# Performance work log

Hardware: AMD Instinct MI355X
Metric: run time of the kernel (lower is better)

## Reference

```python
import jax, jax.numpy as jnp
import numpy as np

B, T, C, H = 4, 4096, 2048, 128


def setup_inputs() -> dict:
    key = jax.random.key(0)
    ks = jax.random.split(key, 7)
    s = 0.02
    return {
        "x": jax.random.normal(ks[0], (B, T, C), dtype=jnp.float32),
        "Wk": jax.random.normal(ks[1], (C, H), dtype=jnp.float32) * s,
        "bk": jax.random.normal(ks[2], (H,), dtype=jnp.float32) * s,
        "Wq": jax.random.normal(ks[3], (C, H), dtype=jnp.float32) * s,
        "bq": jax.random.normal(ks[4], (H,), dtype=jnp.float32) * s,
        "Wv": jax.random.normal(ks[5], (C, H), dtype=jnp.float32) * s,
        "bv": jax.random.normal(ks[6], (H,), dtype=jnp.float32) * s,
    }


def reference(x, Wk, bk, Wq, bq, Wv, bv):
    # x: [B, T, C]
    Bq, Tq, Cq = x.shape
    k = x @ Wk + bk  # [B, T, H]
    q = x @ Wq + bq
    v = x @ Wv + bv
    # NOTE: original scales by C**-0.5 (input emb dim), faithfully reproduced.
    scale = jnp.asarray(Cq, x.dtype) ** -0.5
    wei = jnp.einsum("bth,bsh->bts", q, k) * scale  # [B, T, T]
    causal = jnp.tril(jnp.ones((Tq, Tq), dtype=bool))
    wei = jnp.where(causal, wei, -jnp.inf)
    wei = jax.nn.softmax(wei, axis=-1)
    # dropout omitted (inference/eval mode)
    return jnp.einsum("bts,bsh->bth", wei, v)  # [B, T, H]
```

## Files before the change

kernel.cpp:

```cpp
#include <hip/hip_runtime.h>
#include <hip/hip_bf16.h>
#include <stdint.h>

#define T_SEQ 4096
#define C_DIM 2048
#define H_DIM 128
#define NBATCH 4

typedef unsigned short u16;
typedef __attribute__((ext_vector_type(8))) __bf16 bf16x8;
typedef __attribute__((ext_vector_type(4))) float f32x4;
typedef __attribute__((ext_vector_type(8))) unsigned short u16x8;

__device__ __forceinline__ u16 f2bf(float f) {
  union { float f; uint32_t i; } v; v.f = f;
  uint32_t r = v.i + 0x7FFFu + ((v.i >> 16) & 1u);
  return (u16)(r >> 16);
}

__device__ __forceinline__ void gload16(const void* g, void* l) {
  __builtin_amdgcn_global_load_lds(
      (__attribute__((address_space(1))) void*)(g),
      (__attribute__((address_space(3))) void*)(l), 16, 0, 0);
}

__device__ __forceinline__ f32x4 mfma_bf16(bf16x8 a, bf16x8 b, f32x4 c) {
  return __builtin_amdgcn_mfma_f32_16x16x32_bf16(a, b, c, 0, 0, 0);
}

template<int CTRL>
__device__ __forceinline__ float dpp_mov(float x) {
  return __int_as_float(__builtin_amdgcn_mov_dpp(__float_as_int(x), CTRL, 0xF, 0xF, true));
}
__device__ __forceinline__ float red16_max(float v) {
  v = fmaxf(v, dpp_mov<0x121>(v));
  v = fmaxf(v, dpp_mov<0x122>(v));
  v = fmaxf(v, dpp_mov<0x124>(v));
  v = fmaxf(v, dpp_mov<0x128>(v));
  return v;
}
__device__ __forceinline__ float red16_sum(float v) {
  v += dpp_mov<0x121>(v);
  v += dpp_mov<0x122>(v);
  v += dpp_mov<0x124>(v);
  v += dpp_mov<0x128>(v);
  return v;
}

__global__ __launch_bounds__(256) void transpose_w(
    const float* __restrict__ Wq, const float* __restrict__ Wk,
    const float* __restrict__ Wv, u16* __restrict__ Wt)
{
  __shared__ u16 Wl[64 * 72];
  const int bk = blockIdx.x;
  const int bn = blockIdx.y;
  const int p  = blockIdx.z;
  const float* W = (p == 0) ? Wq : (p == 1) ? Wk : Wv;
  const int t = threadIdx.x;

  for (int ps = 0; ps < 16; ++ps) {
    int e  = ps * 256 + t;
    int kk = e >> 6, nn = e & 63;
    Wl[kk * 72 + nn] = f2bf(W[(size_t)(bk * 64 + kk) * H_DIM + bn * 64 + nn]);
  }
  __syncthreads();
  for (int ps = 0; ps < 16; ++ps) {
    int o  = ps * 256 + t;
    int nl = o >> 6, kl = o & 63;
    int n  = bn * 64 + nl;
    int g  = kl >> 3, j = kl & 7;
    int ks = ((g ^ (n & 7)) << 3) | j;
    Wt[(size_t)p * (H_DIM * C_DIM) + (size_t)n * C_DIM + bk * 64 + kl] = Wl[ks * 72 + nl];
  }
}

__global__ __launch_bounds__(256, 2) void qkv_gemm(
    const float* __restrict__ x, const u16* __restrict__ Wt,
    const float* __restrict__ bq, const float* __restrict__ bk, const float* __restrict__ bv,
    u16* __restrict__ qo, u16* __restrict__ ko, u16* __restrict__ vTo)
{
  __shared__ alignas(16) u16 SMEM[128 * 128];
  u16* As = SMEM;
  u16* Bs = SMEM + 128 * 64;

  const int tid  = threadIdx.x;
  const int w    = tid >> 6, lane = tid & 63;
  const int t16  = lane & 15, quad = lane >> 4;
  const int wr   = w >> 1, wc = w & 1;
  const int rt   = blockIdx.x;
  const int p    = blockIdx.y;

  const u16*   Wp = Wt + (size_t)p * (H_DIM * C_DIM);
  const float* bp = (p == 0) ? bq : (p == 1) ? bk : bv;

  f32x4 acc[4][4];
  for (int i = 0; i < 4; ++i)
    for (int j = 0; j < 4; ++j) acc[i][j] = f32x4{0.f, 0.f, 0.f, 0.f};

  const size_t rowBase = (size_t)rt * 128;

  for (int k0 = 0; k0 < C_DIM; k0 += 64) {
    __syncthreads();
    for (int j = 0; j < 4; ++j) {
      int e8 = (((j << 2) + w) * 64 + lane) * 8;
      int rr = e8 >> 6, kk = e8 & 63;
      gload16(Wp + (size_t)rr * C_DIM + k0 + kk, &Bs[e8]);
    }
    for (int ps = 0; ps < 4; ++ps) {
      int gidx = ps * 256 + tid;
      int row = gidx >> 3, g = gidx & 7;
      const float4* xp = (const float4*)&x[(rowBase + row) * C_DIM + k0 + g * 8];
      float4 a0 = xp[0], a1 = xp[1];
      u16x8 pk;
      pk[0] = f2bf(a0.x); pk[1] = f2bf(a0.y); pk[2] = f2bf(a0.z); pk[3] = f2bf(a0.w);
      pk[4] = f2bf(a1.x); pk[5] = f2bf(a1.y); pk[6] = f2bf(a1.z); pk[7] = f2bf(a1.w);
      *(u16x8*)&As[row * 64 + ((g ^ (row & 7)) << 3)] = pk;
    }
    __syncthreads();
    for (int ks = 0; ks < 2; ++ks) {
      bf16x8 af[4], bfr[4];
      for (int ra = 0; ra < 4; ++ra)
        af[ra] = *(const bf16x8*)&As[(wr * 64 + ra * 16 + t16) * 64 +
                                     (((ks * 4 + quad) ^ (t16 & 7)) << 3)];
      for (int cb = 0; cb < 4; ++cb)
        bfr[cb] = *(const bf16x8*)&Bs[(wc * 64 + cb * 16 + t16) * 64 +
                                      (((ks * 4 + quad) ^ (t16 & 7)) << 3)];
      for (int ra = 0; ra < 4; ++ra)
        for (int cb = 0; cb < 4; ++cb)
          acc[ra][cb] = mfma_bf16(af[ra], bfr[cb], acc[ra][cb]);
    }
  }

  __syncthreads();
  for (int cb = 0; cb < 4; ++cb) {
    int col = wc * 64 + cb * 16 + t16;
    float bias = bp[col];
    for (int ra = 0; ra < 4; ++ra) {
      for (int r = 0; r < 4; ++r) {
        int row16 = wr * 64 + ra * 16 + quad * 4 + r;
        float v = acc[ra][cb][r] + bias;
        if (p == 2) {
          int swz = (row16 >> 3) ^ (col & 15);
          SMEM[col * 128 + (swz << 3) + (row16 & 7)] = f2bf(v);
        } else {
          int g = col >> 3;
          SMEM[row16 * 128 + (((g ^ (row16 & 15)) << 3) | (col & 7))] = f2bf(v);
        }
      }
    }
  }
  __syncthreads();

  if (p == 1) {
    u16* kдst = ko + rowBase * H_DIM;
    for (int ps = 0; ps < 8; ++ps) {
      int c = ps * 256 + tid;
      *(u16x8*)&kдst[c * 8] = *(const u16x8*)&SMEM[c * 8];
    }
  } else if (p == 0) {
    for (int ps = 0; ps < 8; ++ps) {
      int c = ps * 256 + tid;
      int row16 = c >> 4, g = c & 15;
      u16x8 v = *(const u16x8*)&SMEM[row16 * 128 + ((g ^ (row16 & 15)) << 3)];
      *(u16x8*)&qo[(rowBase + row16) * H_DIM + g * 8] = v;
    }
  } else {
    const int bb = rt >> 5;
    const int tb = (rt & 31) * 128;
    for (int ps = 0; ps < 8; ++ps) {
      int c = ps * 256 + tid;
      int d = c >> 4, gt = c & 15;
      u16x8 v = *(const u16x8*)&SMEM[d * 128 + ((gt ^ (d & 15)) << 3)];
      int toff = tb + ((gt >> 3) << 6) + (((gt & 7) ^ (d & 7)) << 3);
      *(u16x8*)&vTo[((size_t)bb * H_DIM + d) * T_SEQ + toff] = v;
    }
  }
}

__global__ __launch_bounds__(256, 2) void flash_attn(
    const u16* __restrict__ q, const u16* __restrict__ k,
    const u16* __restrict__ vT, float* __restrict__ out,
    float* __restrict__ Opart, float* __restrict__ MLpart, int split)
{
  __shared__ alignas(16) u16 Kt[2][64 * 128];
  __shared__ alignas(16) u16 Vt[2][128 * 64];
  __shared__ alignas(16) u16 Ps[4 * 16 * 72];

  const int tid  = threadIdx.x;
  const int w    = tid >> 6, lane = tid & 63;
  const int t16  = lane & 15, quad = lane >> 4;
  const int b    = blockIdx.x;

  int qt, kt0, ktn, slot;
  if (split) {
    int bid = blockIdx.y;
    if (bid < 32)      { qt = 32 + bid; kt0 = 0;  ktn = 32;      slot = (b * 32 + bid) * 2; }
    else if (bid < 64) { qt = 95 - bid; kt0 = 32; ktn = qt - 31; slot = (b * 32 + (qt - 32)) * 2 + 1; }
    else               { qt = 95 - bid; kt0 = 0;  ktn = qt + 1;  slot = -1; }
  } else {
    qt = 63 - blockIdx.y; kt0 = 0; ktn = qt + 1; slot = -1;
  }

  const float SCALE = 0.022097086912079612f;
  const float L2E   = 1.4426950408889634f;

  bf16x8 qf[4];
  {
    const u16* qrow = q + ((size_t)(b * T_SEQ + qt * 64 + w * 16 + t16)) * H_DIM;
    for (int c = 0; c < 4; ++c)
      qf[c] = *(const bf16x8*)(qrow + c * 32 + quad * 8);
  }

  f32x4 Oc[8];
  for (int i = 0; i < 8; ++i) Oc[i] = f32x4{0.f, 0.f, 0.f, 0.f};
  float mrow[4] = {-1e30f, -1e30f, -1e30f, -1e30f};
  float lrow[4] = {0.f, 0.f, 0.f, 0.f};

  const u16* kbase = k  + ((size_t)b * T_SEQ) * H_DIM;
  const u16* vbase = vT + ((size_t)b * H_DIM) * T_SEQ;

  {
    const u16* kg = kbase + (size_t)(kt0 * 64) * H_DIM;
    for (int j = 0; j < 4; ++j) {
      int e8 = (((j << 2) + w) * 64 + lane) * 8;
      gload16(kg + e8, &Kt[0][e8]);
      int d = e8 >> 6, kk = e8 & 63;
      gload16(vbase + (size_t)d * T_SEQ + kt0 * 64 + kk, &Vt[0][e8]);
    }
  }

  int cur = 0;
  for (int it = 0; it < ktn; ++it) {
    const int kt = kt0 + it;
    __syncthreads();
    if (it + 1 < ktn) {
      const int nb = cur ^ 1, ktn1 = kt + 1;
      const u16* kg = kbase + (size_t)(ktn1 * 64) * H_DIM;
      for (int j = 0; j < 4; ++j) {
        int e8 = (((j << 2) + w) * 64 + lane) * 8;
        gload16(kg + e8, &Kt[nb][e8]);
        int d = e8 >> 6, kk = e8 & 63;
        gload16(vbase + (size_t)d * T_SEQ + ktn1 * 64 + kk, &Vt[nb][e8]);
      }
    }

    f32x4 S[4];
    for (int ct = 0; ct < 4; ++ct) S[ct] = f32x4{0.f, 0.f, 0.f, 0.f};
    for (int c = 0; c < 4; ++c) {
      for (int ct = 0; ct < 4; ++ct) {
        bf16x8 kf = *(const bf16x8*)&Kt[cur][(ct * 16 + t16) * H_DIM +
                                            (((c * 4 + quad) ^ t16) << 3)];
        S[ct] = mfma_bf16(qf[c], kf, S[ct]);
      }
    }

    const bool diag = (kt == qt);
    for (int ct = 0; ct < 4; ++ct)
      for (int r = 0; r < 4; ++r) {
        float s = S[ct][r] * SCALE;
        if (diag && (ct * 16 + t16 > w * 16 + quad * 4 + r)) s = -1e30f;
        S[ct][r] = s;
      }

    float alpha[4], mnew[4];
    for (int r = 0; r < 4; ++r) {
      float mx = red16_max(fmaxf(fmaxf(S[0][r], S[1][r]), fmaxf(S[2][r], S[3][r])));
      mnew[r]  = fmaxf(mrow[r], mx);
      alpha[r] = exp2f((mrow[r] - mnew[r]) * L2E);
      mrow[r]  = mnew[r];
    }
    for (int r = 0; r < 4; ++r) {
      float s = 0.f;
      for (int ct = 0; ct < 4; ++ct) {
        float pv = exp2f((S[ct][r] - mnew[r]) * L2E);
        S[ct][r] = pv;
        s += pv;
      }
      lrow[r] = lrow[r] * alpha[r] + red16_sum(s);
    }
    for (int dt = 0; dt < 8; ++dt)
      for (int r = 0; r < 4; ++r)
        Oc[dt][r] *= alpha[r];

    u16* pw = &Ps[w * 1152];
    for (int ct = 0; ct < 4; ++ct)
      for (int r = 0; r < 4; ++r)
        pw[(quad * 4 + r) * 72 + ct * 16 + t16] = f2bf(S[ct][r]);
    __asm__ volatile("s_waitcnt lgkmcnt(0)" ::: "memory");

    for (int ks = 0; ks < 2; ++ks) {
      bf16x8 pf = *(const bf16x8*)&pw[t16 * 72 + ks * 32 + quad * 8];
      for (int dt = 0; dt < 8; ++dt) {
        bf16x8 vf = *(const bf16x8*)&Vt[cur][(dt * 16 + t16) * 64 +
                                            (((ks * 4 + quad) ^ (t16 & 7)) << 3)];
        Oc[dt] = mfma_bf16(pf, vf, Oc[dt]);
      }
    }
    cur ^= 1;
  }

  if (slot < 0) {
    for (int r = 0; r < 4; ++r) {
      float inv = 1.0f / lrow[r];
      size_t row = (size_t)b * T_SEQ + qt * 64 + w * 16 + quad * 4 + r;
      for (int dt = 0; dt < 8; ++dt)
        out[row * H_DIM + dt * 16 + t16] = Oc[dt][r] * inv;
    }
  } else {
    if (t16 == 0) {
      for (int r = 0; r < 4; ++r) {
        int row = w * 16 + quad * 4 + r;
        MLpart[(size_t)slot * 128 + row * 2 + 0] = mrow[r];
        MLpart[(size_t)slot * 128 + row * 2 + 1] = lrow[r];
      }
    }
    float* op = Opart + (size_t)slot * 8192;
    for (int r = 0; r < 4; ++r) {
      int row = w * 16 + quad * 4 + r;
      for (int dt = 0; dt < 8; ++dt)
        op[row * 128 + dt * 16 + t16] = Oc[dt][r];
    }
  }
}

__global__ __launch_bounds__(256) void combine(
    const float* __restrict__ Opart, const float* __restrict__ MLpart,
    float* __restrict__ out)
{
  __shared__ float c1s[64], c2s[64];
  const float L2E = 1.4426950408889634f;
  const int s = blockIdx.x;
  const int b = s >> 5, qt = 32 + (s & 31);
  const int t = threadIdx.x;

  if (t < 64) {
    const float* ML1 = MLpart + (size_t)(s * 2) * 128;
    const float* ML2 = ML1 + 128;
    float m1 = ML1[t * 2], l1 = ML1[t * 2 + 1];
    float m2 = ML2[t * 2], l2 = ML2[t * 2 + 1];
    float m  = fmaxf(m1, m2);
    float e1 = exp2f((m1 - m) * L2E);
    float e2 = exp2f((m2 - m) * L2E);
    float inv = 1.0f / (l1 * e1 + l2 * e2);
    c1s[t] = e1 * inv; c2s[t] = e2 * inv;
  }
  __syncthreads();

  const float* O1 = Opart + (size_t)(s * 2) * 8192;
  const float* O2 = O1 + 8192;
  float* o = out + ((size_t)b * T_SEQ + qt * 64) * (size_t)H_DIM;
  for (int i = t; i < 8192; i += 256) {
    int row = i >> 7;
    o[i] = O1[i] * c1s[row] + O2[i] * c2s[row];
  }
}

extern "C" void kernel_launch(void* const* d_in, const int* in_sizes, int n_in,
                              void* d_out, int out_size, void* d_ws, size_t ws_size,
                              hipStream_t stream) {
  const float* x  = (const float*)d_in[0];
  const float* Wk = (const float*)d_in[1];
  const float* bk = (const float*)d_in[2];
  const float* Wq = (const float*)d_in[3];
  const float* bq = (const float*)d_in[4];
  const float* Wv = (const float*)d_in[5];
  const float* bv = (const float*)d_in[6];
  float* out = (float*)d_out;

  char* ws = (char*)d_ws;
  u16* qb  = (u16*)(ws);
  u16* kb  = (u16*)(ws + 4194304);
  u16* vT  = (u16*)(ws + 8388608);
  u16* Wt  = (u16*)(ws + 12582912);
  float* Opart  = (float*)(ws + 14155776);
  float* MLpart = (float*)(ws + 14155776 + 8388608);

  const size_t need = 14155776ull + 8388608ull + 131072ull;
  const int split = (ws_size >= need) ? 1 : 0;

  hipLaunchKernelGGL(transpose_w, dim3(32, 2, 3), dim3(256), 0, stream, Wq, Wk, Wv, Wt);
  hipLaunchKernelGGL(qkv_gemm, dim3(128, 3), dim3(256), 0, stream,
                     x, Wt, bq, bk, bv, qb, kb, vT);
  hipLaunchKernelGGL(flash_attn, dim3(4, split ? 96 : 64), dim3(256), 0, stream,
                     qb, kb, vT, out, Opart, MLpart, split);
  if (split)
    hipLaunchKernelGGL(combine, dim3(128), dim3(256), 0, stream, Opart, MLpart, out);
}
```

Baseline: 324.3 us.

## Fuse Q/K/V projections into one GEMM sharing each x tile

```diff
diff --git a/kernel.cpp b/kernel.cpp
--- a/kernel.cpp
+++ b/kernel.cpp
@@ -74,105 +74,113 @@
   }
 }
 
-__global__ __launch_bounds__(256, 2) void qkv_gemm(
+__global__ __launch_bounds__(512, 2) void qkv_fused(
     const float* __restrict__ x, const u16* __restrict__ Wt,
     const float* __restrict__ bq, const float* __restrict__ bk, const float* __restrict__ bv,
     u16* __restrict__ qo, u16* __restrict__ ko, u16* __restrict__ vTo)
 {
-  __shared__ alignas(16) u16 SMEM[128 * 128];
+  __shared__ alignas(16) u16 SMEM[28672];
   u16* As = SMEM;
-  u16* Bs = SMEM + 128 * 64;
+  u16* Bs = SMEM + 4096;
 
   const int tid  = threadIdx.x;
   const int w    = tid >> 6, lane = tid & 63;
   const int t16  = lane & 15, quad = lane >> 4;
-  const int wr   = w >> 1, wc = w & 1;
+  const int mh   = w >> 2;
+  const int nq   = w & 3;
   const int rt   = blockIdx.x;
-  const int p    = blockIdx.y;
-
-  const u16*   Wp = Wt + (size_t)p * (H_DIM * C_DIM);
-  const float* bp = (p == 0) ? bq : (p == 1) ? bk : bv;
-
-  f32x4 acc[4][4];
-  for (int i = 0; i < 4; ++i)
-    for (int j = 0; j < 4; ++j) acc[i][j] = f32x4{0.f, 0.f, 0.f, 0.f};
-
-  const size_t rowBase = (size_t)rt * 128;
+
+  f32x4 acc[2][6];
+  for (int i = 0; i < 2; ++i)
+    for (int j = 0; j < 6; ++j) acc[i][j] = f32x4{0.f, 0.f, 0.f, 0.f};
+
+  const size_t rowBase = (size_t)rt * 64;
+  const int arow = tid >> 3;
+  const int ag   = tid & 7;
+  const float* xrow = &x[(rowBase + arow) * C_DIM + ag * 8];
+
+  float4 a0 = ((const float4*)xrow)[0];
+  float4 a1 = ((const float4*)xrow)[1];
 
   for (int k0 = 0; k0 < C_DIM; k0 += 64) {
     __syncthreads();
-    for (int j = 0; j < 4; ++j) {
-      int e8 = (((j << 2) + w) * 64 + lane) * 8;
-      int rr = e8 >> 6, kk = e8 & 63;
-      gload16(Wp + (size_t)rr * C_DIM + k0 + kk, &Bs[e8]);
-    }
-    for (int ps = 0; ps < 4; ++ps) {
-      int gidx = ps * 256 + tid;
-      int row = gidx >> 3, g = gidx & 7;
-      const float4* xp = (const float4*)&x[(rowBase + row) * C_DIM + k0 + g * 8];
-      float4 a0 = xp[0], a1 = xp[1];
+    for (int p = 0; p < 3; ++p) {
+      const u16* Wp = Wt + (size_t)p * (H_DIM * C_DIM);
+      for (int j = 0; j < 2; ++j) {
+        int e8 = (((j << 3) + w) * 64 + lane) * 8;
+        int rr = e8 >> 6, kk = e8 & 63;
+        gload16(Wp + (size_t)rr * C_DIM + k0 + kk, &Bs[p * 8192 + e8]);
+      }
+    }
+    {
       u16x8 pk;
       pk[0] = f2bf(a0.x); pk[1] = f2bf(a0.y); pk[2] = f2bf(a0.z); pk[3] = f2bf(a0.w);
       pk[4] = f2bf(a1.x); pk[5] = f2bf(a1.y); pk[6] = f2bf(a1.z); pk[7] = f2bf(a1.w);
-      *(u16x8*)&As[row * 64 + ((g ^ (row & 7)) << 3)] = pk;
+      *(u16x8*)&As[arow * 64 + ((ag ^ (arow & 7)) << 3)] = pk;
+    }
+    if (k0 + 64 < C_DIM) {
+      const float4* xp = (const float4*)(xrow + k0 + 64);
+      a0 = xp[0]; a1 = xp[1];
     }
     __syncthreads();
+
     for (int ks = 0; ks < 2; ++ks) {
-      bf16x8 af[4], bfr[4];
-      for (int ra = 0; ra < 4; ++ra)
-        af[ra] = *(const bf16x8*)&As[(wr * 64 + ra * 16 + t16) * 64 +
+      bf16x8 af[2], bfr[6];
+      for (int ra = 0; ra < 2; ++ra)
+        af[ra] = *(const bf16x8*)&As[(mh * 32 + ra * 16 + t16) * 64 +
                                      (((ks * 4 + quad) ^ (t16 & 7)) << 3)];
-      for (int cb = 0; cb < 4; ++cb)
-        bfr[cb] = *(const bf16x8*)&Bs[(wc * 64 + cb * 16 + t16) * 64 +
-                                      (((ks * 4 + quad) ^ (t16 & 7)) << 3)];
-      for (int ra = 0; ra < 4; ++ra)
-        for (int cb = 0; cb < 4; ++cb)
-          acc[ra][cb] = mfma_bf16(af[ra], bfr[cb], acc[ra][cb]);
+      for (int c = 0; c < 6; ++c) {
+        int col = nq * 96 + c * 16 + t16;
+        int p = col >> 7, pc = col & 127;
+        bfr[c] = *(const bf16x8*)&Bs[p * 8192 + pc * 64 +
+                                     (((ks * 4 + quad) ^ (t16 & 7)) << 3)];
+      }
+      for (int ra = 0; ra < 2; ++ra)
+        for (int c = 0; c < 6; ++c)
+          acc[ra][c] = mfma_bf16(af[ra], bfr[c], acc[ra][c]);
     }
   }
 
   __syncthreads();
-  for (int cb = 0; cb < 4; ++cb) {
-    int col = wc * 64 + cb * 16 + t16;
-    float bias = bp[col];
-    for (int ra = 0; ra < 4; ++ra) {
+  u16* Oq = SMEM;
+  u16* Ok = SMEM + 8192;
+  u16* Ov = SMEM + 16384;
+
+  for (int c = 0; c < 6; ++c) {
+    int col = nq * 96 + c * 16 + t16;
+    int p = col >> 7, pc = col & 127;
+    float bias = (p == 0) ? bq[pc] : (p == 1) ? bk[pc] : bv[pc];
+    for (int ra = 0; ra < 2; ++ra) {
       for (int r = 0; r < 4; ++r) {
-        int row16 = wr * 64 + ra * 16 + quad * 4 + r;
-        float v = acc[ra][cb][r] + bias;
+        int row16 = mh * 32 + ra * 16 + quad * 4 + r;
+        float v = acc[ra][c][r] + bias;
         if (p == 2) {
-          int swz = (row16 >> 3) ^ (col & 15);
-          SMEM[col * 128 + (swz << 3) + (row16 & 7)] = f2bf(v);
+          int gt = row16 >> 3;
+          Ov[pc * 64 + ((gt ^ (pc & 7)) << 3) + (row16 & 7)] = f2bf(v);
         } else {
-          int g = col >> 3;
-          SMEM[row16 * 128 + (((g ^ (row16 & 15)) << 3) | (col & 7))] = f2bf(v);
+          u16* O = (p == 0) ? Oq : Ok;
+          int g = pc >> 3;
+          O[row16 * 128 + (((g ^ (row16 & 15)) << 3) | (pc & 7))] = f2bf(v);
         }
       }
     }
   }
   __syncthreads();
 
-  if (p == 1) {
-    u16* kдst = ko + rowBase * H_DIM;
-    for (int ps = 0; ps < 8; ++ps) {
-      int c = ps * 256 + tid;
-      *(u16x8*)&kдst[c * 8] = *(const u16x8*)&SMEM[c * 8];
-    }
-  } else if (p == 0) {
-    for (int ps = 0; ps < 8; ++ps) {
-      int c = ps * 256 + tid;
+  const int bb = rt >> 6;
+  const int tb = (rt & 63) * 64;
+  for (int ps = 0; ps < 2; ++ps) {
+    int c = ps * 512 + tid;
+    {
       int row16 = c >> 4, g = c & 15;
-      u16x8 v = *(const u16x8*)&SMEM[row16 * 128 + ((g ^ (row16 & 15)) << 3)];
+      u16x8 v = *(const u16x8*)&Oq[row16 * 128 + ((g ^ (row16 & 15)) << 3)];
       *(u16x8*)&qo[(rowBase + row16) * H_DIM + g * 8] = v;
     }
-  } else {
-    const int bb = rt >> 5;
-    const int tb = (rt & 31) * 128;
-    for (int ps = 0; ps < 8; ++ps) {
-      int c = ps * 256 + tid;
-      int d = c >> 4, gt = c & 15;
-      u16x8 v = *(const u16x8*)&SMEM[d * 128 + ((gt ^ (d & 15)) << 3)];
-      int toff = tb + ((gt >> 3) << 6) + (((gt & 7) ^ (d & 7)) << 3);
-      *(u16x8*)&vTo[((size_t)bb * H_DIM + d) * T_SEQ + toff] = v;
+    *(u16x8*)&ko[rowBase * H_DIM + c * 8] = *(const u16x8*)&Ok[c * 8];
+    {
+      int d = c >> 3, gc = c & 7;
+      *(u16x8*)&vTo[((size_t)bb * H_DIM + d) * T_SEQ + tb + gc * 8] =
+          *(const u16x8*)&Ov[c * 8];
     }
   }
 }
@@ -379,7 +387,7 @@
   const int split = (ws_size >= need) ? 1 : 0;
 
   hipLaunchKernelGGL(transpose_w, dim3(32, 2, 3), dim3(256), 0, stream, Wq, Wk, Wv, Wt);
-  hipLaunchKernelGGL(qkv_gemm, dim3(128, 3), dim3(256), 0, stream,
+  hipLaunchKernelGGL(qkv_fused, dim3(256), dim3(512), 0, stream,
                      x, Wt, bq, bk, bv, qb, kb, vT);
   hipLaunchKernelGGL(flash_attn, dim3(4, split ? 96 : 64), dim3(256), 0, stream,
                      qb, kb, vT, out, Opart, MLpart, split);
```

Result: faster. 310.4 us (-4.3%).
